# Performance work log

Hardware: AMD Instinct MI355X
Metric: run time of the kernel (lower is better)

The kernel has to match this reference:

```python
import jax, jax.numpy as jnp
import numpy as np

N, E = 50000, 800000
IN, HID, H, OUT, ED = 128, 16, 4, 7, 2
HC = HID * H  # 64


def setup_inputs() -> dict:
    key = jax.random.key(0)
    ks = jax.random.split(key, 24)
    g = lambda k, s, sc=0.05: (jax.random.normal(k, s, dtype=jnp.float32) * sc)
    return {
        'x': g(ks[0], (N, IN), 1.0),
        'edge_attr': g(ks[1], (E, ED), 1.0),
        'edge_index': jax.random.randint(ks[2], (2, E), 0, N),
        # conv1: in=IN, out=HID, heads=H, edge_dim=ED, concat=True
        'Wq1': g(ks[3], (IN, HC)), 'bq1': jnp.zeros((HC,), jnp.float32),
        'Wk1': g(ks[4], (IN, HC)), 'bk1': jnp.zeros((HC,), jnp.float32),
        'Wv1': g(ks[5], (IN, HC)), 'bv1': jnp.zeros((HC,), jnp.float32),
        'We1': g(ks[6], (ED, HC)),  # lin_edge has no bias in PyG
        'Ws1': g(ks[7], (IN, HC)), 'bs1': jnp.zeros((HC,), jnp.float32),
        # conv2: in=HC, out=OUT, heads=1, concat=False
        'Wq2': g(ks[8], (HC, OUT)), 'bq2': jnp.zeros((OUT,), jnp.float32),
        'Wk2': g(ks[9], (HC, OUT)), 'bk2': jnp.zeros((OUT,), jnp.float32),
        'Wv2': g(ks[10], (HC, OUT)), 'bv2': jnp.zeros((OUT,), jnp.float32),
        'Ws2': g(ks[11], (HC, OUT)), 'bs2': jnp.zeros((OUT,), jnp.float32),
    }


def transformer_conv(x, src, dst, Wq, bq, Wk, bk, Wv, bv, Ws, bs,
                     heads, ch, concat, edge_attr=None, We=None):
    """PyG TransformerConv (eval mode, root_weight=True, beta=False)."""
    n = x.shape[0]
    q = (x @ Wq + bq).reshape(n, heads, ch)
    k = (x @ Wk + bk).reshape(n, heads, ch)
    v = (x @ Wv + bv).reshape(n, heads, ch)
    kj = k[src]  # [E,H,C] gather from source nodes
    vj = v[src]
    if We is not None:
        e = (edge_attr @ We).reshape(-1, heads, ch)
        kj = kj + e
        vj = vj + e
    # per-edge attention logits [E,H]
    alpha = (q[dst] * kj).sum(-1) / jnp.sqrt(jnp.float32(ch))
    # scatter-softmax over incoming edges of each destination node
    amax = jax.ops.segment_max(alpha, dst, num_segments=n)
    ex = jnp.exp(alpha - amax[dst])
    denom = jax.ops.segment_sum(ex, dst, num_segments=n)
    a = ex / jnp.maximum(denom, 1e-16)[dst]
    out = jax.ops.segment_sum(vj * a[:, :, None], dst, num_segments=n)  # [N,H,C]
    out = out.reshape(n, heads * ch) if concat else out.mean(axis=1)
    return out + x @ Ws + bs  # skip connection (lin_skip)


def reference(x, edge_attr, edge_index, Wq1, bq1, Wk1, bk1, Wv1, bv1, We1,
              Ws1, bs1, Wq2, bq2, Wk2, bk2, Wv2, bv2, Ws2, bs2):
    src, dst = edge_index[0], edge_index[1]
    # eval mode: feature/attention dropout are identity
    h = transformer_conv(x, src, dst, Wq1, bq1, Wk1, bk1, Wv1, bv1, Ws1, bs1,
                         H, HID, True, edge_attr=edge_attr, We=We1)
    h = jax.nn.elu(h)
    out = transformer_conv(h, src, dst, Wq2, bq2, Wk2, bk2, Wv2, bv2, Ws2, bs2,
                           1, OUT, False)
    return out
```

## Files before the change

### kernel.cpp

```cpp
#include <hip/hip_runtime.h>


#define N_NODES 50000
#define N_EDGES 800000
#define IN_F    128
#define HC      64
#define NH      4
#define CH      16
#define OUTF    7

#define DPB 100
#define NBK (N_NODES / DPB)
#define SC_EPB 4096
#define SCA_BLOCKS ((N_EDGES + SC_EPB - 1) / SC_EPB)

typedef __attribute__((ext_vector_type(8))) short bf16x8;
typedef __attribute__((ext_vector_type(4))) float f32x4;

__device__ __forceinline__ unsigned short f2bf(float f) {
    unsigned u = __float_as_uint(f);
    unsigned r = u + 0x7FFFu + ((u >> 16) & 1u);
    return (unsigned short)(r >> 16);
}
__device__ __forceinline__ float bflo(unsigned u) { return __uint_as_float(u << 16); }
__device__ __forceinline__ float bfhi(unsigned u) { return __uint_as_float(u & 0xFFFF0000u); }

__device__ __forceinline__ float dpp_add4(float x) {
    int t;
    t = __builtin_amdgcn_update_dpp(0, __float_as_int(x), 0xB1, 0xF, 0xF, false);
    x += __int_as_float(t);
    t = __builtin_amdgcn_update_dpp(0, __float_as_int(x), 0x4E, 0xF, 0xF, false);
    x += __int_as_float(t);
    return x;
}
__device__ __forceinline__ float dpp_add16(float x) {
    int t;
    t = __builtin_amdgcn_update_dpp(0, __float_as_int(x), 0xB1, 0xF, 0xF, false);
    x += __int_as_float(t);
    t = __builtin_amdgcn_update_dpp(0, __float_as_int(x), 0x4E, 0xF, 0xF, false);
    x += __int_as_float(t);
    t = __builtin_amdgcn_update_dpp(0, __float_as_int(x), 0x124, 0xF, 0xF, false);
    x += __int_as_float(t);
    t = __builtin_amdgcn_update_dpp(0, __float_as_int(x), 0x128, 0xF, 0xF, false);
    x += __int_as_float(t);
    return x;
}
__device__ __forceinline__ float dpp_max16(float x) {
    int t;
    t = __builtin_amdgcn_update_dpp(0, __float_as_int(x), 0xB1, 0xF, 0xF, false);
    x = fmaxf(x, __int_as_float(t));
    t = __builtin_amdgcn_update_dpp(0, __float_as_int(x), 0x4E, 0xF, 0xF, false);
    x = fmaxf(x, __int_as_float(t));
    t = __builtin_amdgcn_update_dpp(0, __float_as_int(x), 0x124, 0xF, 0xF, false);
    x = fmaxf(x, __int_as_float(t));
    t = __builtin_amdgcn_update_dpp(0, __float_as_int(x), 0x128, 0xF, 0xF, false);
    x = fmaxf(x, __int_as_float(t));
    return x;
}

__global__ __launch_bounds__(256) void convert_w_kernel(
    const float* __restrict__ Wq, const float* __restrict__ Wk,
    const float* __restrict__ Wv, const float* __restrict__ Ws,
    unsigned short* __restrict__ Wt, int* __restrict__ bcnt)
{
    int i = blockIdx.x * 256 + threadIdx.x;
    if (blockIdx.x < 2) {
        int j = blockIdx.x * 256 + threadIdx.x;
        if (j < NBK) bcnt[j] = 0;
    }
    if (i >= 4 * HC * IN_F) return;
    int m   = i >> 13;
    int col = (i >> 7) & 63;
    int k   = i & 127;
    const float* W = (m == 0) ? Wq : (m == 1) ? Wk : (m == 2) ? Wv : Ws;
    Wt[i] = f2bf(W[k * HC + col]);
}

__global__ __launch_bounds__(256) void proj1_mfma_kernel(
    const float* __restrict__ x, const unsigned short* __restrict__ Wt,
    const float* __restrict__ bq, const float* __restrict__ bk,
    const float* __restrict__ bv, const float* __restrict__ bs,
    float* __restrict__ q1, unsigned short* __restrict__ kv1,
    float* __restrict__ s1)
{
    __shared__ unsigned short xs[16][136];
    const int t = threadIdx.x;
    const int w = t >> 6, lane = t & 63;
    const int n0 = blockIdx.x * 16;
    const int col16 = lane & 15, kg = lane >> 4;

    bf16x8 bfrag[4][4];
#pragma unroll
    for (int tt = 0; tt < 4; tt++) {
        const unsigned short* bp = Wt + ((size_t)(w * 64 + tt * 16 + col16) * IN_F) + 8 * kg;
#pragma unroll
        for (int kc = 0; kc < 4; kc++)
            bfrag[kc][tt] = *(const bf16x8*)(bp + kc * 32);
    }

    {
        int row = t >> 4, k8 = (t & 15) * 8;
        const float* xp = x + (size_t)(n0 + row) * IN_F + k8;
        float4 f0 = *(const float4*)xp;
        float4 f1 = *(const float4*)(xp + 4);
        uint4 pk;
        pk.x = f2bf(f0.x) | ((unsigned)f2bf(f0.y) << 16);
        pk.y = f2bf(f0.z) | ((unsigned)f2bf(f0.w) << 16);
        pk.z = f2bf(f1.x) | ((unsigned)f2bf(f1.y) << 16);
        pk.w = f2bf(f1.z) | ((unsigned)f2bf(f1.w) << 16);
        *(uint4*)&xs[row][k8] = pk;
    }
    __syncthreads();

    f32x4 acc[4] = { {0,0,0,0}, {0,0,0,0}, {0,0,0,0}, {0,0,0,0} };
#pragma unroll
    for (int kc = 0; kc < 4; kc++) {
        bf16x8 a = *(const bf16x8*)&xs[col16][kc * 32 + 8 * kg];
#pragma unroll
        for (int tt = 0; tt < 4; tt++)
            acc[tt] = __builtin_amdgcn_mfma_f32_16x16x32_bf16(a, bfrag[kc][tt], acc[tt], 0, 0, 0);
    }

    if (w == 0 || w == 3) {
        const float* Bm = (w == 0) ? bq : bs;
        float*       Om = (w == 0) ? q1 : s1;
#pragma unroll
        for (int tt = 0; tt < 4; tt++) {
            int col = tt * 16 + col16;
            float bias = Bm[col];
#pragma unroll
            for (int r = 0; r < 4; r++) {
                int node = n0 + kg * 4 + r;
                Om[(size_t)node * HC + col] = acc[tt][r] + bias;
            }
        }
    } else {
        const float* Bm = (w == 1) ? bk : bv;
        const int cbase = (w == 1) ? 0 : 64;
#pragma unroll
        for (int tt = 0; tt < 4; tt++) {
            int col = tt * 16 + col16;
            float bias = Bm[col];
#pragma unroll
            for (int r = 0; r < 4; r++) {
                int node = n0 + kg * 4 + r;
                kv1[(size_t)node * 128 + cbase + col] = f2bf(acc[tt][r] + bias);
            }
        }
    }
}

__global__ __launch_bounds__(256) void bhist_kernel(
    const int* __restrict__ ei, int* __restrict__ bcnt)
{
    __shared__ int cnt[NBK];
    const int t = threadIdx.x;
    const int e0 = blockIdx.x * SC_EPB;
    const int e1 = (e0 + SC_EPB < N_EDGES) ? e0 + SC_EPB : N_EDGES;
    for (int j = t; j < NBK; j += 256) cnt[j] = 0;
    __syncthreads();
    for (int e = e0 + t; e < e1; e += 256)
        atomicAdd(&cnt[ei[N_EDGES + e] / DPB], 1);
    __syncthreads();
    for (int j = t; j < NBK; j += 256)
        if (cnt[j]) atomicAdd(&bcnt[j], cnt[j]);
}

__global__ __launch_bounds__(256) void bscan_kernel(
    const int* __restrict__ bcnt, int* __restrict__ bofs2, int* __restrict__ bcur)
{
    __shared__ int partial[256];
    const int t = threadIdx.x;
    const int b0 = t * 2;
    int c0 = (b0     < NBK) ? bcnt[b0]     : 0;
    int c1 = (b0 + 1 < NBK) ? bcnt[b0 + 1] : 0;
    int s = c0 + c1;
    partial[t] = s;
    __syncthreads();
    for (int d = 1; d < 256; d <<= 1) {
        int u = (t >= d) ? partial[t - d] : 0;
        __syncthreads();
        partial[t] += u;
        __syncthreads();
    }
    int run = partial[t] - s;
    if (b0 < NBK)     { bofs2[b0]     = run;      bcur[b0]     = run; }
    if (b0 + 1 < NBK) { bofs2[b0 + 1] = run + c0; bcur[b0 + 1] = run + c0; }
    if (t == 255) bofs2[NBK] = N_EDGES;
}

__global__ __launch_bounds__(256) void scatterA_kernel(
    const int* __restrict__ ei, const float* __restrict__ ea,
    int* __restrict__ bcur, uint2* __restrict__ etmp)
{
    __shared__ int cnt[NBK];
    __shared__ int base[NBK];
    const int t = threadIdx.x;
    const int e0 = blockIdx.x * SC_EPB;
    const int e1 = (e0 + SC_EPB < N_EDGES) ? e0 + SC_EPB : N_EDGES;

    for (int j = t; j < NBK; j += 256) cnt[j] = 0;
    __syncthreads();
    for (int e = e0 + t; e < e1; e += 256)
        atomicAdd(&cnt[ei[N_EDGES + e] / DPB], 1);
    __syncthreads();
    for (int j = t; j < NBK; j += 256) {
        int c = cnt[j];
        if (c) base[j] = atomicAdd(&bcur[j], c);
        cnt[j] = 0;
    }
    __syncthreads();
    for (int e = e0 + t; e < e1; e += 256) {
        int d = ei[N_EDGES + e];
        int s = ei[e];
        int b = d / DPB;
        int li = atomicAdd(&cnt[b], 1);
        uint2 r;
        r.x = (unsigned)s | ((unsigned)d << 16);
        r.y = (unsigned)f2bf(ea[(size_t)e * 2])
            | ((unsigned)f2bf(ea[(size_t)e * 2 + 1]) << 16);
        etmp[base[b] + li] = r;
    }
}

__global__ __launch_bounds__(256) void sortB_kernel(
    const int* __restrict__ bofs2, const uint2* __restrict__ etmp,
    uint2* __restrict__ erec, int* __restrict__ offs)
{
    __shared__ int deg[DPB];
    __shared__ int pre[DPB];
    __shared__ int cur[DPB];
    const int t = threadIdx.x;
    const int b = blockIdx.x;
    const int dlo = b * DPB;
    const int rbeg = bofs2[b], rend = bofs2[b + 1];

    if (t < DPB) deg[t] = 0;
    __syncthreads();
    for (int i = rbeg + t; i < rend; i += 256)
        atomicAdd(&deg[(int)(etmp[i].x >> 16) - dlo], 1);
    __syncthreads();
    if (t < DPB) pre[t] = deg[t];
    __syncthreads();
#pragma unroll
    for (int d = 1; d < DPB; d <<= 1) {
        int u = (t >= d && t < DPB) ? pre[t - d] : 0;
        __syncthreads();
        if (t < DPB) pre[t] += u;
        __syncthreads();
    }
    if (t < DPB) {
        int o = rbeg + pre[t] - deg[t];
        offs[dlo + t] = o;
        cur[t] = o;
    }
    if (b == NBK - 1 && t == 0) offs[N_NODES] = N_EDGES;
    __syncthreads();
    for (int i = rbeg + t; i < rend; i += 256) {
        uint2 r = etmp[i];
        int d = (int)(r.x >> 16) - dlo;
        int pos = atomicAdd(&cur[d], 1);
        uint2 o;
        o.x = r.x & 0xFFFFu;
        o.y = r.y;
        erec[pos] = o;
    }
}

__global__ __launch_bounds__(256) void attn1_kernel(
    const int* __restrict__ offs, const uint2* __restrict__ erec,
    const float* __restrict__ We,
    const float* __restrict__ q1, const unsigned short* __restrict__ kv1,
    const float* __restrict__ s1, float* __restrict__ h)
{
    int n    = (blockIdx.x * 256 + threadIdx.x) >> 6;
    int lane = threadIdx.x & 63;
    if (n >= N_NODES) return;
    const int g = lane >> 4;
    const int s = lane & 15;

    const float4 qv  = *(const float4*)(q1 + (size_t)n * HC + s * 4);
    const float4 We0 = *(const float4*)(We + s * 4);
    const float4 We1 = *(const float4*)(We + HC + s * 4);

    float qw0 = dpp_add4(qv.x*We0.x + qv.y*We0.y + qv.z*We0.z + qv.w*We0.w);
    float qw1 = dpp_add4(qv.x*We1.x + qv.y*We1.y + qv.z*We1.z + qv.w*We1.w);

    const int beg = offs[n], end = offs[n + 1];
    float m = -3.402823466e38f, l = 0.f, A0 = 0.f, A1 = 0.f;
    float4 acc = make_float4(0.f, 0.f, 0.f, 0.f);

    for (int base = beg; base < end; base += 4) {
        int i = base + g;
        bool valid = (i < end);
        uint2 r = erec[valid ? i : beg];
        int src = (int)r.x;
        float ea0 = bflo(r.y), ea1 = bfhi(r.y);
        const unsigned short* kvp = kv1 + ((size_t)src << 7) + (s << 2);
        uint2 kraw = *(const uint2*)kvp;
        uint2 vraw = *(const uint2*)(kvp + 64);
        float k0 = bflo(kraw.x), k1 = bfhi(kraw.x);
        float k2 = bflo(kraw.y), k3 = bfhi(kraw.y);
        float dot = qv.x*k0 + qv.y*k1 + qv.z*k2 + qv.w*k3;
        dot = dpp_add4(dot);
        float logit = valid ? (dot + ea0 * qw0 + ea1 * qw1) * 0.25f
                            : -3.402823466e38f;
        if (__any(logit > m + 8.f)) {
            float mn = fmaxf(m, logit);
            float sm = __expf(m - mn);
            l *= sm; A0 *= sm; A1 *= sm;
            acc.x *= sm; acc.y *= sm; acc.z *= sm; acc.w *= sm;
            m = mn;
        }
        float pe = valid ? __expf(logit - m) : 0.f;
        l += pe;
        float v0 = bflo(vraw.x), v1 = bfhi(vraw.x);
        float v2 = bflo(vraw.y), v3 = bfhi(vraw.y);
        acc.x += pe * v0; acc.y += pe * v1;
        acc.z += pe * v2; acc.w += pe * v3;
        A0 += pe * ea0;  A1 += pe * ea1;
    }

    if (end > beg) {
        float M = fmaxf(m, __shfl_xor(m, 16));
        M = fmaxf(M, __shfl_xor(M, 32));
        float sc = __expf(m - M);
        l *= sc; A0 *= sc; A1 *= sc;
        acc.x *= sc; acc.y *= sc; acc.z *= sc; acc.w *= sc;
        l  += __shfl_xor(l, 16);   l  += __shfl_xor(l, 32);
        A0 += __shfl_xor(A0, 16);  A0 += __shfl_xor(A0, 32);
        A1 += __shfl_xor(A1, 16);  A1 += __shfl_xor(A1, 32);
        acc.x += __shfl_xor(acc.x, 16); acc.x += __shfl_xor(acc.x, 32);
        acc.y += __shfl_xor(acc.y, 16); acc.y += __shfl_xor(acc.y, 32);
        acc.z += __shfl_xor(acc.z, 16); acc.z += __shfl_xor(acc.z, 32);
        acc.w += __shfl_xor(acc.w, 16); acc.w += __shfl_xor(acc.w, 32);
        if (lane < 16) {
            float inv = 1.f / l;
            float4 sk = *(const float4*)(s1 + (size_t)n * HC + s * 4);
            float4 o;
            o.x = (acc.x + A0 * We0.x + A1 * We1.x) * inv + sk.x;
            o.y = (acc.y + A0 * We0.y + A1 * We1.y) * inv + sk.y;
            o.z = (acc.z + A0 * We0.z + A1 * We1.z) * inv + sk.z;
            o.w = (acc.w + A0 * We0.w + A1 * We1.w) * inv + sk.w;
            o.x = o.x > 0.f ? o.x : expm1f(o.x);
            o.y = o.y > 0.f ? o.y : expm1f(o.y);
            o.z = o.z > 0.f ? o.z : expm1f(o.z);
            o.w = o.w > 0.f ? o.w : expm1f(o.w);
            *(float4*)(h + (size_t)n * HC + s * 4) = o;
        }
    } else if (lane < 16) {
        float4 sk = *(const float4*)(s1 + (size_t)n * HC + s * 4);
        float4 o;
        o.x = sk.x > 0.f ? sk.x : expm1f(sk.x);
        o.y = sk.y > 0.f ? sk.y : expm1f(sk.y);
        o.z = sk.z > 0.f ? sk.z : expm1f(sk.z);
        o.w = sk.w > 0.f ? sk.w : expm1f(sk.w);
        *(float4*)(h + (size_t)n * HC + s * 4) = o;
    }
}

__global__ __launch_bounds__(256) void proj2_kernel(
    const float* __restrict__ h,
    const float* __restrict__ Wq, const float* __restrict__ bq,
    const float* __restrict__ Wk, const float* __restrict__ bk,
    const float* __restrict__ Wv, const float* __restrict__ bv,
    const float* __restrict__ Ws, const float* __restrict__ bs,
    float* __restrict__ q2p, float* __restrict__ kv2, float* __restrict__ s2p)
{
    __shared__ float Wsm[HC][4][8];
    __shared__ float Bsm[4][8];
    const int t = threadIdx.x;

    for (int j = t; j < HC * 28; j += 256) {
        int i = j / 28, r = j % 28, mtx = r / 7, c = r % 7;
        const float* W = (mtx == 0) ? Wq : (mtx == 1) ? Wk : (mtx == 2) ? Wv : Ws;
        Wsm[i][mtx][c] = W[i * OUTF + c];
    }
    for (int j = t; j < HC * 4; j += 256)
        Wsm[j >> 2][j & 3][7] = 0.f;
    if (t < 32) {
        int mtx = t >> 3, c = t & 7;
        const float* B = (mtx == 0) ? bq : (mtx == 1) ? bk : (mtx == 2) ? bv : bs;
        Bsm[mtx][c] = (c < 7) ? B[c] : 0.f;
    }
    __syncthreads();

    int n = blockIdx.x * 256 + t;
    if (n >= N_NODES) return;

    float acc[4][8];
#pragma unroll
    for (int mtx = 0; mtx < 4; mtx++)
#pragma unroll
        for (int c = 0; c < 8; c++) acc[mtx][c] = Bsm[mtx][c];

    const float4* hp = (const float4*)(h + (size_t)n * HC);
#pragma unroll 4
    for (int i4 = 0; i4 < 16; i4++) {
        float4 hv = hp[i4];
        float hx[4] = { hv.x, hv.y, hv.z, hv.w };
#pragma unroll
        for (int e = 0; e < 4; e++) {
            int i = i4 * 4 + e;
#pragma unroll
            for (int mtx = 0; mtx < 4; mtx++) {
                float4 wa = *(const float4*)&Wsm[i][mtx][0];
                float4 wb = *(const float4*)&Wsm[i][mtx][4];
                acc[mtx][0] += hx[e] * wa.x; acc[mtx][1] += hx[e] * wa.y;
                acc[mtx][2] += hx[e] * wa.z; acc[mtx][3] += hx[e] * wa.w;
                acc[mtx][4] += hx[e] * wb.x; acc[mtx][5] += hx[e] * wb.y;
                acc[mtx][6] += hx[e] * wb.z; acc[mtx][7] += hx[e] * wb.w;
            }
        }
    }

    float4* q2v = (float4*)(q2p + (size_t)n * 8);
    q2v[0] = make_float4(acc[0][0], acc[0][1], acc[0][2], acc[0][3]);
    q2v[1] = make_float4(acc[0][4], acc[0][5], acc[0][6], acc[0][7]);
    float4* kvv = (float4*)(kv2 + (size_t)n * 16);
    kvv[0] = make_float4(acc[1][0], acc[1][1], acc[1][2], acc[1][3]);
    kvv[1] = make_float4(acc[1][4], acc[1][5], acc[1][6], acc[1][7]);
    kvv[2] = make_float4(acc[2][0], acc[2][1], acc[2][2], acc[2][3]);
    kvv[3] = make_float4(acc[2][4], acc[2][5], acc[2][6], acc[2][7]);
    float4* s2v = (float4*)(s2p + (size_t)n * 8);
    s2v[0] = make_float4(acc[3][0], acc[3][1], acc[3][2], acc[3][3]);
    s2v[1] = make_float4(acc[3][4], acc[3][5], acc[3][6], acc[3][7]);
}

__global__ __launch_bounds__(256) void attn2_kernel(
    const int* __restrict__ offs, const uint2* __restrict__ erec,
    const float* __restrict__ q2p, const float* __restrict__ kv2,
    const float* __restrict__ s2p, float* __restrict__ out)
{
    int idx = blockIdx.x * 256 + threadIdx.x;
    int n   = idx >> 4;
    int s   = idx & 15;
    if (n >= N_NODES) return;

    float4 qa = *(const float4*)(q2p + (size_t)n * 8);
    float4 qb = *(const float4*)(q2p + (size_t)n * 8 + 4);
    int beg = offs[n], end = offs[n + 1];

    float m = -3.402823466e38f, l = 0.f, a[OUTF];
#pragma unroll
    for (int c = 0; c < OUTF; c++) a[c] = 0.f;

    for (int i = beg + s; i < end; i += 16) {
        int src = (int)erec[i].x;
        const float4* kvp = (const float4*)(kv2 + (size_t)src * 16);
        float4 ka = kvp[0], kb = kvp[1], va = kvp[2], vb = kvp[3];
        float dot = qa.x * ka.x + qa.y * ka.y + qa.z * ka.z + qa.w * ka.w
                  + qb.x * kb.x + qb.y * kb.y + qb.z * kb.z;
        float logit = dot * 0.37796447300922725f;
        float mn = fmaxf(m, logit);
        float sc = __expf(m - mn);
        float pe = __expf(logit - mn);
        l = l * sc + pe;
        a[0] = a[0] * sc + pe * va.x;
        a[1] = a[1] * sc + pe * va.y;
        a[2] = a[2] * sc + pe * va.z;
        a[3] = a[3] * sc + pe * va.w;
        a[4] = a[4] * sc + pe * vb.x;
        a[5] = a[5] * sc + pe * vb.y;
        a[6] = a[6] * sc + pe * vb.z;
        m = mn;
    }

    if (end > beg) {
        float M = dpp_max16(m);
        float sc = __expf(m - M);
        l *= sc;
#pragma unroll
        for (int c = 0; c < OUTF; c++) a[c] *= sc;
        l = dpp_add16(l);
#pragma unroll
        for (int c = 0; c < OUTF; c++) a[c] = dpp_add16(a[c]);
        if (s == 0) {
            float inv = 1.f / fmaxf(l, 1e-16f);
#pragma unroll
            for (int c = 0; c < OUTF; c++)
                out[(size_t)n * OUTF + c] = a[c] * inv + s2p[(size_t)n * 8 + c];
        }
    } else if (s == 0) {
#pragma unroll
        for (int c = 0; c < OUTF; c++)
            out[(size_t)n * OUTF + c] = s2p[(size_t)n * 8 + c];
    }
}

extern "C" void kernel_launch(void* const* d_in, const int* in_sizes, int n_in,
                              void* d_out, int out_size, void* d_ws, size_t ws_size,
                              hipStream_t stream)
{
    const float* x    = (const float*)d_in[0];
    const float* ea   = (const float*)d_in[1];
    const int*   ei   = (const int*)d_in[2];
    const float* Wq1  = (const float*)d_in[3];
    const float* bq1  = (const float*)d_in[4];
    const float* Wk1  = (const float*)d_in[5];
    const float* bk1  = (const float*)d_in[6];
    const float* Wv1  = (const float*)d_in[7];
    const float* bv1  = (const float*)d_in[8];
    const float* We1  = (const float*)d_in[9];
    const float* Ws1  = (const float*)d_in[10];
    const float* bs1  = (const float*)d_in[11];
    const float* Wq2  = (const float*)d_in[12];
    const float* bq2  = (const float*)d_in[13];
    const float* Wk2  = (const float*)d_in[14];
    const float* bk2  = (const float*)d_in[15];
    const float* Wv2  = (const float*)d_in[16];
    const float* bv2  = (const float*)d_in[17];
    const float* Ws2  = (const float*)d_in[18];
    const float* bs2  = (const float*)d_in[19];
    float* out = (float*)d_out;

    float* ws = (float*)d_ws;
    float*          q1  = ws;
    float*          s1  = q1 + (size_t)N_NODES * HC;
    unsigned short* kv1 = (unsigned short*)(s1 + (size_t)N_NODES * HC);
    float*          hbuf = q1;
    uint2* erec = (uint2*)((float*)kv1 + (size_t)N_NODES * HC);
    uint2* etmp = erec + N_EDGES;
    float*  q2p  = (float*)(etmp + N_EDGES);
    float*  kv2  = q2p + (size_t)N_NODES * 8;
    float*  s2p  = kv2 + (size_t)N_NODES * 16;
    unsigned short* Wt = (unsigned short*)(s2p + (size_t)N_NODES * 8);
    int*    offs  = (int*)(Wt + 4 * HC * IN_F);
    int*    bcnt  = offs + N_NODES + 1;
    int*    bofs2 = bcnt + NBK;
    int*    bcur  = bofs2 + NBK + 1;

    convert_w_kernel<<<(4 * HC * IN_F + 255) / 256, 256, 0, stream>>>(
        Wq1, Wk1, Wv1, Ws1, Wt, bcnt);

    proj1_mfma_kernel<<<N_NODES / 16, 256, 0, stream>>>(
        x, Wt, bq1, bk1, bv1, bs1, q1, kv1, s1);

    bhist_kernel<<<SCA_BLOCKS, 256, 0, stream>>>(ei, bcnt);
    bscan_kernel<<<1, 256, 0, stream>>>(bcnt, bofs2, bcur);
    scatterA_kernel<<<SCA_BLOCKS, 256, 0, stream>>>(ei, ea, bcur, etmp);
    sortB_kernel<<<NBK, 256, 0, stream>>>(bofs2, etmp, erec, offs);

    attn1_kernel<<<(N_NODES * 64 + 255) / 256, 256, 0, stream>>>(
        offs, erec, We1, q1, kv1, s1, hbuf);

    proj2_kernel<<<(N_NODES + 255) / 256, 256, 0, stream>>>(
        hbuf, Wq2, bq2, Wk2, bk2, Wv2, bv2, Ws2, bs2, q2p, kv2, s2p);

    attn2_kernel<<<(N_NODES * 16 + 255) / 256, 256, 0, stream>>>(
        offs, erec, q2p, kv2, s2p, out);
}
```

Measured before the change: 152.3 us.

## Merge layer-1 projection with edge scatter in one launch; use fast ELU

The layer-1 MFMA projection and the bucket-scatter pass now run in a single kernel launch. Block indices past the projection range run the scatter, so the two independent workloads can share the GPU and one launch plus its pipeline drain are removed. The kernel grows by about 4 KB of shared memory for the scatter counters, which may lower occupancy for the projection blocks. ELU also switches from expm1f to __expf(x)-1, which is cheaper but slightly less accurate near zero.

Result: faster. 145.6 us (-4.4%).

```diff
diff --git a/kernel.cpp b/kernel.cpp
--- a/kernel.cpp
+++ b/kernel.cpp
@@ -13,6 +13,7 @@
 #define NBK (N_NODES / DPB)
 #define SC_EPB 4096
 #define SCA_BLOCKS ((N_EDGES + SC_EPB - 1) / SC_EPB)
+#define P1_BLOCKS (N_NODES / 16)
 
 typedef __attribute__((ext_vector_type(8))) short bf16x8;
 typedef __attribute__((ext_vector_type(4))) float f32x4;
@@ -24,6 +25,9 @@
 }
 __device__ __forceinline__ float bflo(unsigned u) { return __uint_as_float(u << 16); }
 __device__ __forceinline__ float bfhi(unsigned u) { return __uint_as_float(u & 0xFFFF0000u); }
+__device__ __forceinline__ float elu_fast(float x) {
+    return x > 0.f ? x : __expf(x) - 1.f;
+}
 
 __device__ __forceinline__ float dpp_add4(float x) {
     int t;
@@ -76,15 +80,87 @@
     Wt[i] = f2bf(W[k * HC + col]);
 }
 
-__global__ __launch_bounds__(256) void proj1_mfma_kernel(
+__global__ __launch_bounds__(256) void bhist_kernel(
+    const int* __restrict__ ei, int* __restrict__ bcnt)
+{
+    __shared__ int cnt[NBK];
+    const int t = threadIdx.x;
+    const int e0 = blockIdx.x * SC_EPB;
+    const int e1 = (e0 + SC_EPB < N_EDGES) ? e0 + SC_EPB : N_EDGES;
+    for (int j = t; j < NBK; j += 256) cnt[j] = 0;
+    __syncthreads();
+    for (int e = e0 + t; e < e1; e += 256)
+        atomicAdd(&cnt[ei[N_EDGES + e] / DPB], 1);
+    __syncthreads();
+    for (int j = t; j < NBK; j += 256)
+        if (cnt[j]) atomicAdd(&bcnt[j], cnt[j]);
+}
+
+__global__ __launch_bounds__(256) void bscan_kernel(
+    const int* __restrict__ bcnt, int* __restrict__ bofs2, int* __restrict__ bcur)
+{
+    __shared__ int partial[256];
+    const int t = threadIdx.x;
+    const int b0 = t * 2;
+    int c0 = (b0     < NBK) ? bcnt[b0]     : 0;
+    int c1 = (b0 + 1 < NBK) ? bcnt[b0 + 1] : 0;
+    int s = c0 + c1;
+    partial[t] = s;
+    __syncthreads();
+    for (int d = 1; d < 256; d <<= 1) {
+        int u = (t >= d) ? partial[t - d] : 0;
+        __syncthreads();
+        partial[t] += u;
+        __syncthreads();
+    }
+    int run = partial[t] - s;
+    if (b0 < NBK)     { bofs2[b0]     = run;      bcur[b0]     = run; }
+    if (b0 + 1 < NBK) { bofs2[b0 + 1] = run + c0; bcur[b0 + 1] = run + c0; }
+    if (t == 255) bofs2[NBK] = N_EDGES;
+}
+
+__global__ __launch_bounds__(256) void proj1_scatterA_kernel(
     const float* __restrict__ x, const unsigned short* __restrict__ Wt,
     const float* __restrict__ bq, const float* __restrict__ bk,
     const float* __restrict__ bv, const float* __restrict__ bs,
     float* __restrict__ q1, unsigned short* __restrict__ kv1,
-    float* __restrict__ s1)
+    float* __restrict__ s1,
+    const int* __restrict__ ei, const float* __restrict__ ea,
+    int* __restrict__ bcur, uint2* __restrict__ etmp)
 {
     __shared__ unsigned short xs[16][136];
+    __shared__ int cnt[NBK];
+    __shared__ int base[NBK];
     const int t = threadIdx.x;
+
+    if (blockIdx.x >= P1_BLOCKS) {
+        const int e0 = (blockIdx.x - P1_BLOCKS) * SC_EPB;
+        const int e1 = (e0 + SC_EPB < N_EDGES) ? e0 + SC_EPB : N_EDGES;
+        for (int j = t; j < NBK; j += 256) cnt[j] = 0;
+        __syncthreads();
+        for (int e = e0 + t; e < e1; e += 256)
+            atomicAdd(&cnt[ei[N_EDGES + e] / DPB], 1);
+        __syncthreads();
+        for (int j = t; j < NBK; j += 256) {
+            int c = cnt[j];
+            if (c) base[j] = atomicAdd(&bcur[j], c);
+            cnt[j] = 0;
+        }
+        __syncthreads();
+        for (int e = e0 + t; e < e1; e += 256) {
+            int d = ei[N_EDGES + e];
+            int s = ei[e];
+            int b = d / DPB;
+            int li = atomicAdd(&cnt[b], 1);
+            uint2 r;
+            r.x = (unsigned)s | ((unsigned)d << 16);
+            r.y = (unsigned)f2bf(ea[(size_t)e * 2])
+                | ((unsigned)f2bf(ea[(size_t)e * 2 + 1]) << 16);
+            etmp[base[b] + li] = r;
+        }
+        return;
+    }
+
     const int w = t >> 6, lane = t & 63;
     const int n0 = blockIdx.x * 16;
     const int col16 = lane & 15, kg = lane >> 4;
@@ -147,79 +223,6 @@
                 kv1[(size_t)node * 128 + cbase + col] = f2bf(acc[tt][r] + bias);
             }
         }
-    }
-}
-
-__global__ __launch_bounds__(256) void bhist_kernel(
-    const int* __restrict__ ei, int* __restrict__ bcnt)
-{
-    __shared__ int cnt[NBK];
-    const int t = threadIdx.x;
-    const int e0 = blockIdx.x * SC_EPB;
-    const int e1 = (e0 + SC_EPB < N_EDGES) ? e0 + SC_EPB : N_EDGES;
-    for (int j = t; j < NBK; j += 256) cnt[j] = 0;
-    __syncthreads();
-    for (int e = e0 + t; e < e1; e += 256)
-        atomicAdd(&cnt[ei[N_EDGES + e] / DPB], 1);
-    __syncthreads();
-    for (int j = t; j < NBK; j += 256)
-        if (cnt[j]) atomicAdd(&bcnt[j], cnt[j]);
-}
-
-__global__ __launch_bounds__(256) void bscan_kernel(
-    const int* __restrict__ bcnt, int* __restrict__ bofs2, int* __restrict__ bcur)
-{
-    __shared__ int partial[256];
-    const int t = threadIdx.x;
-    const int b0 = t * 2;
-    int c0 = (b0     < NBK) ? bcnt[b0]     : 0;
-    int c1 = (b0 + 1 < NBK) ? bcnt[b0 + 1] : 0;
-    int s = c0 + c1;
-    partial[t] = s;
-    __syncthreads();
-    for (int d = 1; d < 256; d <<= 1) {
-        int u = (t >= d) ? partial[t - d] : 0;
-        __syncthreads();
-        partial[t] += u;
-        __syncthreads();
-    }
-    int run = partial[t] - s;
-    if (b0 < NBK)     { bofs2[b0]     = run;      bcur[b0]     = run; }
-    if (b0 + 1 < NBK) { bofs2[b0 + 1] = run + c0; bcur[b0 + 1] = run + c0; }
-    if (t == 255) bofs2[NBK] = N_EDGES;
-}
-
-__global__ __launch_bounds__(256) void scatterA_kernel(
-    const int* __restrict__ ei, const float* __restrict__ ea,
-    int* __restrict__ bcur, uint2* __restrict__ etmp)
-{
-    __shared__ int cnt[NBK];
-    __shared__ int base[NBK];
-    const int t = threadIdx.x;
-    const int e0 = blockIdx.x * SC_EPB;
-    const int e1 = (e0 + SC_EPB < N_EDGES) ? e0 + SC_EPB : N_EDGES;
-
-    for (int j = t; j < NBK; j += 256) cnt[j] = 0;
-    __syncthreads();
-    for (int e = e0 + t; e < e1; e += 256)
-        atomicAdd(&cnt[ei[N_EDGES + e] / DPB], 1);
-    __syncthreads();
-    for (int j = t; j < NBK; j += 256) {
-        int c = cnt[j];
-        if (c) base[j] = atomicAdd(&bcur[j], c);
-        cnt[j] = 0;
-    }
-    __syncthreads();
-    for (int e = e0 + t; e < e1; e += 256) {
-        int d = ei[N_EDGES + e];
-        int s = ei[e];
-        int b = d / DPB;
-        int li = atomicAdd(&cnt[b], 1);
-        uint2 r;
-        r.x = (unsigned)s | ((unsigned)d << 16);
-        r.y = (unsigned)f2bf(ea[(size_t)e * 2])
-            | ((unsigned)f2bf(ea[(size_t)e * 2 + 1]) << 16);
-        etmp[base[b] + li] = r;
     }
 }
 
@@ -338,23 +341,19 @@
             float inv = 1.f / l;
             float4 sk = *(const float4*)(s1 + (size_t)n * HC + s * 4);
             float4 o;
-            o.x = (acc.x + A0 * We0.x + A1 * We1.x) * inv + sk.x;
-            o.y = (acc.y + A0 * We0.y + A1 * We1.y) * inv + sk.y;
-            o.z = (acc.z + A0 * We0.z + A1 * We1.z) * inv + sk.z;
-            o.w = (acc.w + A0 * We0.w + A1 * We1.w) * inv + sk.w;
-            o.x = o.x > 0.f ? o.x : expm1f(o.x);
-            o.y = o.y > 0.f ? o.y : expm1f(o.y);
-            o.z = o.z > 0.f ? o.z : expm1f(o.z);
-            o.w = o.w > 0.f ? o.w : expm1f(o.w);
+            o.x = elu_fast((acc.x + A0 * We0.x + A1 * We1.x) * inv + sk.x);
+            o.y = elu_fast((acc.y + A0 * We0.y + A1 * We1.y) * inv + sk.y);
+            o.z = elu_fast((acc.z + A0 * We0.z + A1 * We1.z) * inv + sk.z);
+            o.w = elu_fast((acc.w + A0 * We0.w + A1 * We1.w) * inv + sk.w);
             *(float4*)(h + (size_t)n * HC + s * 4) = o;
         }
     } else if (lane < 16) {
         float4 sk = *(const float4*)(s1 + (size_t)n * HC + s * 4);
         float4 o;
-        o.x = sk.x > 0.f ? sk.x : expm1f(sk.x);
-        o.y = sk.y > 0.f ? sk.y : expm1f(sk.y);
-        o.z = sk.z > 0.f ? sk.z : expm1f(sk.z);
-        o.w = sk.w > 0.f ? sk.w : expm1f(sk.w);
+        o.x = elu_fast(sk.x);
+        o.y = elu_fast(sk.y);
+        o.z = elu_fast(sk.z);
+        o.w = elu_fast(sk.w);
         *(float4*)(h + (size_t)n * HC + s * 4) = o;
     }
 }
@@ -533,12 +532,12 @@
     convert_w_kernel<<<(4 * HC * IN_F + 255) / 256, 256, 0, stream>>>(
         Wq1, Wk1, Wv1, Ws1, Wt, bcnt);
 
-    proj1_mfma_kernel<<<N_NODES / 16, 256, 0, stream>>>(
-        x, Wt, bq1, bk1, bv1, bs1, q1, kv1, s1);
-
     bhist_kernel<<<SCA_BLOCKS, 256, 0, stream>>>(ei, bcnt);
     bscan_kernel<<<1, 256, 0, stream>>>(bcnt, bofs2, bcur);
-    scatterA_kernel<<<SCA_BLOCKS, 256, 0, stream>>>(ei, ea, bcur, etmp);
+
+    proj1_scatterA_kernel<<<P1_BLOCKS + SCA_BLOCKS, 256, 0, stream>>>(
+        x, Wt, bq1, bk1, bv1, bs1, q1, kv1, s1, ei, ea, bcur, etmp);
+
     sortB_kernel<<<NBK, 256, 0, stream>>>(bofs2, etmp, erec, offs);
 
     attn1_kernel<<<(N_NODES * 64 + 255) / 256, 256, 0, stream>>>(
```
